# Kernel tuning notes

Measured on AMD Instinct MI355X. Metric: run time of the kernel, lower is better.

Reference implementation:

```python
import jax, jax.numpy as jnp
import numpy as np

E, D, O, G, H, K = 8, 1024, 1024, 512, 2048, 2
B = 8192

def _xavier(key, shape):
    fan_in, fan_out = shape[-2], shape[-1]
    lim = float(np.sqrt(6.0 / (fan_in + fan_out)))
    return jax.random.uniform(key, shape, jnp.float32, -lim, lim)

def setup_inputs() -> dict:
    key = jax.random.key(0)
    ks = jax.random.split(key, 6)
    x = jax.random.normal(ks[0], (B, D), jnp.float32)
    # stacked expert params (xavier-uniform weights, zero bias like torch init)
    W1 = _xavier(ks[1], (E, D, H))
    b1 = jnp.zeros((E, H), jnp.float32)
    W2 = _xavier(ks[2], (E, H, O))
    b2 = jnp.zeros((E, O), jnp.float32)
    # gate params
    Wg1 = _xavier(ks[3], (D, G))
    bg1 = jnp.zeros((G,), jnp.float32)
    Wg2 = _xavier(ks[4], (G, E))
    bg2 = jnp.zeros((E,), jnp.float32)
    return {"x": x, "W1": W1, "b1": b1, "W2": W2, "b2": b2,
            "Wg1": Wg1, "bg1": bg1, "Wg2": Wg2, "bg2": bg2}

def reference(x, W1, b1, W2, b2, Wg1, bg1, Wg2, bg2):
    batch = x.shape[0]
    # gate (dropout inactive in eval)
    gate_logits = jax.nn.relu(x @ Wg1 + bg1) @ Wg2 + bg2          # [B,E]
    gate_scores = jax.nn.softmax(gate_logits, axis=1)
    top_k_scores, top_k_indices = jax.lax.top_k(gate_scores, K)   # [B,K]
    # dense all-expert MLP (mirrors torch.stack over experts)
    h = jax.nn.relu(jnp.einsum('bd,edh->ebh', x, W1) + b1[:, None, :])   # [E,B,H]
    expert_outputs = jnp.einsum('ebh,eho->beo', h, W2) + b2[None, :, :]  # [B,E,O]
    # gather top-k expert outputs, scale, combine
    selected = jnp.take_along_axis(expert_outputs, top_k_indices[:, :, None], axis=1)  # [B,K,O]
    scaled = selected * top_k_scores[:, :, None]
    scaled = scaled / (jnp.sum(top_k_scores, axis=1, keepdims=True)[:, :, None] + 1e-9)
    combined = jnp.sum(scaled, axis=1)                            # [B,O]
    # auxiliary loss
    one_hot = jax.nn.one_hot(top_k_indices, E, dtype=jnp.float32) # [B,K,E]
    expert_load = jnp.sum(one_hot, axis=(0, 1)) / (batch + 1e-9)
    load_balancing_loss = jnp.var(expert_load, ddof=1)            # torch var is unbiased
    entropy = -jnp.mean(jnp.sum(gate_scores * jnp.log(gate_scores + 1e-9), axis=1))
    aux_loss = load_balancing_loss + entropy
    return combined, aux_loss
```

## Files before the change

### kernel.cpp

```cpp
#include <hip/hip_runtime.h>

#define B_ 8192
#define D_ 1024
#define O_ 1024
#define G_ 512
#define H_ 2048
#define E_ 8
#define ROWSP (B_ * 2 + E_ * 128)
#define TAU 0.01f

typedef unsigned short u16;
using f32x4 = __attribute__((ext_vector_type(4))) float;
using s16x8 = __attribute__((ext_vector_type(8))) short;

__device__ __forceinline__ u16 f2bf(float f) {
  union { float f; unsigned u; } v; v.f = f;
  unsigned r = v.u + 0x7FFFu + ((v.u >> 16) & 1u);
  return (u16)(r >> 16);
}
__device__ __forceinline__ float bf2f(u16 h) {
  union { unsigned u; float f; } v; v.u = ((unsigned)h) << 16; return v.f;
}
__device__ __forceinline__ void gload16(const void* g, void* l) {
  __builtin_amdgcn_global_load_lds(
      (const __attribute__((address_space(1))) unsigned int*)g,
      (__attribute__((address_space(3))) unsigned int*)l, 16, 0, 0);
}
__device__ __forceinline__ int xcd_swz(int bid, int nwg) {
  return (bid & 7) * (nwg >> 3) + (bid >> 3);
}
__device__ __forceinline__ int stage_kc(int t) {
  return (((t & 3) ^ ((t >> 3) & 3)) * 8);
}
__device__ __forceinline__ int frag_idx(int lane, int i) {
  int row = i * 16 + (lane & 15);
  int s = (lane >> 4) ^ ((lane >> 1) & 3);
  return (row * 4 + s) * 8;
}

#define PREP_CAST_BLK (B_ * D_ / 4 / 256)
#define PREP_WG1_BLK  ((G_ / 32) * (D_ / 32))
#define PREP_W1_BLK   ((H_ / 32) * (D_ / 32) * E_)
#define PREP_W2_BLK   ((O_ / 32) * (H_ / 32) * E_)

__device__ __forceinline__ void tr_cast_tile(const float* __restrict__ src,
                                             u16* __restrict__ dhi,
                                             u16* __restrict__ dlo,
                                             int R, int C, int bx, int by,
                                             float (*tile)[33], int t) {
  int tx = t & 31, ty = t >> 5;
  int c0 = bx * 32, r0 = by * 32;
#pragma unroll
  for (int p = 0; p < 4; ++p) {
    int r = ty + p * 8;
    tile[r][tx] = src[(size_t)(r0 + r) * C + c0 + tx];
  }
  __syncthreads();
#pragma unroll
  for (int p = 0; p < 4; ++p) {
    int r = ty + p * 8;
    float v = tile[tx][r];
    size_t o = (size_t)(c0 + r) * R + r0 + tx;
    dhi[o] = f2bf(v);
    if (dlo) dlo[o] = f2bf(v - bf2f(f2bf(v)));
  }
}

__global__ __launch_bounds__(256) void k_prep(const float* __restrict__ x,
                                              u16* __restrict__ xhi, u16* __restrict__ xlo,
                                              const float* __restrict__ Wg1,
                                              u16* __restrict__ wg1h, u16* __restrict__ wg1l,
                                              const float* __restrict__ W1, u16* __restrict__ w1t,
                                              const float* __restrict__ W2, u16* __restrict__ w2t) {
  __shared__ float tile[32][33];
  int t = threadIdx.x;
  int b = blockIdx.x;
  if (b < PREP_CAST_BLK) {
    int i = b * 256 + t;
    float4 v = ((const float4*)x)[i];
    u16 h0 = f2bf(v.x), h1 = f2bf(v.y), h2 = f2bf(v.z), h3 = f2bf(v.w);
    ushort4 hi; hi.x = h0; hi.y = h1; hi.z = h2; hi.w = h3;
    ushort4 lo;
    lo.x = f2bf(v.x - bf2f(h0)); lo.y = f2bf(v.y - bf2f(h1));
    lo.z = f2bf(v.z - bf2f(h2)); lo.w = f2bf(v.w - bf2f(h3));
    ((ushort4*)xhi)[i] = hi; ((ushort4*)xlo)[i] = lo;
    return;
  }
  b -= PREP_CAST_BLK;
  if (b < PREP_WG1_BLK) {
    tr_cast_tile(Wg1, wg1h, wg1l, D_, G_, b & 15, b >> 4, tile, t);
    return;
  }
  b -= PREP_WG1_BLK;
  if (b < PREP_W1_BLK) {
    int e = b >> 11, rr = b & 2047;
    size_t ofs = (size_t)e * D_ * H_;
    tr_cast_tile(W1 + ofs, w1t + ofs, nullptr, D_, H_, rr & 63, rr >> 6, tile, t);
    return;
  }
  b -= PREP_W1_BLK;
  {
    int e = b >> 11, rr = b & 2047;
    size_t ofs = (size_t)e * H_ * O_;
    tr_cast_tile(W2 + ofs, w2t + ofs, nullptr, H_, O_, rr & 31, rr >> 5, tile, t);
  }
}

__global__ __launch_bounds__(256) void k_gate_gemm1(const u16* __restrict__ xhi,
                                                    const u16* __restrict__ xlo,
                                                    const u16* __restrict__ whi,
                                                    const u16* __restrict__ wlo,
                                                    const float* __restrict__ bg1,
                                                    float* __restrict__ G1) {
  __shared__ u16 Ah[4096], Al[4096], Bh[4096], Bl[4096];
  int work = xcd_swz(blockIdx.x, (G_ / 128) * (B_ / 128));
  int m0 = (work >> 2) * 128, n0 = (work & 3) * 128;
  int t = threadIdx.x;
  int wave = t >> 6, lane = t & 63;
  int wm = wave >> 1, wn = wave & 1;

  const f32x4 z = {0.f, 0.f, 0.f, 0.f};
  f32x4 acc[4][4];
#pragma unroll
  for (int i = 0; i < 4; ++i)
#pragma unroll
    for (int j = 0; j < 4; ++j) acc[i][j] = z;

  int ar = t >> 2, ac = stage_kc(t);
  const u16* xh0 = xhi + (size_t)(m0 + ar) * D_ + ac;
  const u16* xh1 = xhi + (size_t)(m0 + 64 + ar) * D_ + ac;
  const u16* xl0 = xlo + (size_t)(m0 + ar) * D_ + ac;
  const u16* xl1 = xlo + (size_t)(m0 + 64 + ar) * D_ + ac;
  const u16* wh0 = whi + (size_t)(n0 + ar) * D_ + ac;
  const u16* wh1 = whi + (size_t)(n0 + 64 + ar) * D_ + ac;
  const u16* wl0 = wlo + (size_t)(n0 + ar) * D_ + ac;
  const u16* wl1 = wlo + (size_t)(n0 + 64 + ar) * D_ + ac;

  for (int k0 = 0; k0 < D_; k0 += 32) {
    gload16(xh0 + k0, &Ah[t * 8]); gload16(xh1 + k0, &Ah[2048 + t * 8]);
    gload16(xl0 + k0, &Al[t * 8]); gload16(xl1 + k0, &Al[2048 + t * 8]);
    gload16(wh0 + k0, &Bh[t * 8]); gload16(wh1 + k0, &Bh[2048 + t * 8]);
    gload16(wl0 + k0, &Bl[t * 8]); gload16(wl1 + k0, &Bl[2048 + t * 8]);
    __syncthreads();
    s16x8 ah[4], al[4], bh[4], bl[4];
#pragma unroll
    for (int i = 0; i < 4; ++i) {
      ah[i] = *(const s16x8*)&Ah[wm * 2048 + frag_idx(lane, i)];
      al[i] = *(const s16x8*)&Al[wm * 2048 + frag_idx(lane, i)];
      bh[i] = *(const s16x8*)&Bh[wn * 2048 + frag_idx(lane, i)];
      bl[i] = *(const s16x8*)&Bl[wn * 2048 + frag_idx(lane, i)];
    }
#pragma unroll
    for (int i = 0; i < 4; ++i)
#pragma unroll
      for (int j = 0; j < 4; ++j) {
        acc[i][j] = __builtin_amdgcn_mfma_f32_16x16x32_bf16(ah[i], bh[j], acc[i][j], 0, 0, 0);
        acc[i][j] = __builtin_amdgcn_mfma_f32_16x16x32_bf16(ah[i], bl[j], acc[i][j], 0, 0, 0);
        acc[i][j] = __builtin_amdgcn_mfma_f32_16x16x32_bf16(al[i], bh[j], acc[i][j], 0, 0, 0);
      }
    __syncthreads();
  }
#pragma unroll
  for (int j = 0; j < 4; ++j) {
    int col = n0 + wn * 64 + j * 16 + (lane & 15);
    float bias = bg1[col];
#pragma unroll
    for (int i = 0; i < 4; ++i)
#pragma unroll
      for (int q = 0; q < 4; ++q) {
        int row = m0 + wm * 64 + i * 16 + (lane >> 4) * 4 + q;
        float v = acc[i][j][q] + bias;
        G1[(size_t)row * G_ + col] = v > 0.f ? v : 0.f;
      }
  }
}

__global__ __launch_bounds__(256) void k_gate_logits(const float* __restrict__ G1,
                                                     const float* __restrict__ Wg2,
                                                     const float* __restrict__ bg2,
                                                     float* __restrict__ logits,
                                                     int* __restrict__ flaglist,
                                                     int* __restrict__ nflag) {
  int t = threadIdx.x, wave = t >> 6, lane = t & 63;
  int row = blockIdx.x * 4 + wave;

  float4 g0 = *(const float4*)(G1 + (size_t)row * G_ + lane * 8);
  float4 g1 = *(const float4*)(G1 + (size_t)row * G_ + lane * 8 + 4);
  float g[8] = {g0.x, g0.y, g0.z, g0.w, g1.x, g1.y, g1.z, g1.w};
  float p[8] = {0, 0, 0, 0, 0, 0, 0, 0};
#pragma unroll
  for (int cc = 0; cc < 8; ++cc) {
    int c = lane * 8 + cc;
    float4 w0 = *(const float4*)(Wg2 + c * 8);
    float4 w1 = *(const float4*)(Wg2 + c * 8 + 4);
    p[0] += g[cc] * w0.x; p[1] += g[cc] * w0.y; p[2] += g[cc] * w0.z; p[3] += g[cc] * w0.w;
    p[4] += g[cc] * w1.x; p[5] += g[cc] * w1.y; p[6] += g[cc] * w1.z; p[7] += g[cc] * w1.w;
  }
#pragma unroll
  for (int off = 32; off >= 1; off >>= 1)
#pragma unroll
    for (int e = 0; e < 8; ++e) p[e] += __shfl_xor(p[e], off);
  if (lane == 0) {
    float l1 = -1e30f, l2 = -1e30f, l3 = -1e30f;
#pragma unroll
    for (int e = 0; e < 8; ++e) {
      float v = p[e] + bg2[e];
      logits[(size_t)row * 8 + e] = v;
      if (v > l1) { l3 = l2; l2 = l1; l1 = v; }
      else if (v > l2) { l3 = l2; l2 = v; }
      else if (v > l3) { l3 = v; }
    }
    if (l2 - l3 < TAU) {
      int pos = atomicAdd(nflag, 1);
      flaglist[pos] = row;
    }
  }
}

__global__ __launch_bounds__(256) void k_gate_fixup(const float* __restrict__ x,
                                                    const float* __restrict__ Wg1,
                                                    const float* __restrict__ bg1,
                                                    const float* __restrict__ Wg2,
                                                    const float* __restrict__ bg2,
                                                    const int* __restrict__ flaglist,
                                                    const int* __restrict__ nflag,
                                                    float* __restrict__ logits) {
  __shared__ float xs[1024];
  __shared__ float red[256][9];
  int t = threadIdx.x;
  int n = *nflag;
  for (int i = blockIdx.x; i < n; i += gridDim.x) {
    int row = flaglist[i];
    ((float4*)xs)[t] = ((const float4*)(x + (size_t)row * D_))[t];
    __syncthreads();
    int c0 = t * 2;
    float h0 = 0.f, h1 = 0.f;
#pragma unroll 8
    for (int d = 0; d < D_; ++d) {
      float xv = xs[d];
      float2 w = *(const float2*)(Wg1 + (size_t)d * G_ + c0);
      h0 += xv * w.x; h1 += xv * w.y;
    }
    h0 += bg1[c0]; h1 += bg1[c0 + 1];
    h0 = h0 > 0.f ? h0 : 0.f; h1 = h1 > 0.f ? h1 : 0.f;
#pragma unroll
    for (int e = 0; e < 8; ++e)
      red[t][e] = h0 * Wg2[c0 * 8 + e] + h1 * Wg2[(c0 + 1) * 8 + e];
    __syncthreads();
    for (int s = 128; s >= 1; s >>= 1) {
      if (t < s) {
#pragma unroll
        for (int e = 0; e < 8; ++e) red[t][e] += red[t + s][e];
      }
      __syncthreads();
    }
    if (t < 8) logits[(size_t)row * 8 + t] = red[0][t] + bg2[t];
    __syncthreads();
  }
}

__global__ __launch_bounds__(256) void k_gate_final(const float* __restrict__ logits,
                                                    int* __restrict__ topidx,
                                                    float* __restrict__ wnorm,
                                                    int* __restrict__ counts,
                                                    float* __restrict__ entacc) {
  __shared__ int cnt_s[8];
  __shared__ float ent_s[4];
  int t = threadIdx.x;
  if (t < 8) cnt_s[t] = 0;
  __syncthreads();
  int row = blockIdx.x * 256 + t;
  float4 a = ((const float4*)logits)[(size_t)row * 2];
  float4 b = ((const float4*)logits)[(size_t)row * 2 + 1];
  float L[8] = {a.x, a.y, a.z, a.w, b.x, b.y, b.z, b.w};
  float m = L[0];
#pragma unroll
  for (int e = 1; e < 8; ++e) m = fmaxf(m, L[e]);
  float s[8], Z = 0.f;
#pragma unroll
  for (int e = 0; e < 8; ++e) { s[e] = expf(L[e] - m); Z += s[e]; }
  float inv = 1.f / Z;
  float sc[8];
#pragma unroll
  for (int e = 0; e < 8; ++e) sc[e] = s[e] * inv;
  int i1 = 0;
#pragma unroll
  for (int e = 1; e < 8; ++e) if (L[e] > L[i1]) i1 = e;
  int i2 = (i1 == 0) ? 1 : 0;
#pragma unroll
  for (int e = 0; e < 8; ++e) if (e != i1 && L[e] > L[i2]) i2 = e;
  float s1 = sc[i1], s2 = sc[i2];
  float denom = s1 + s2 + 1e-9f;
  topidx[row * 2] = i1; topidx[row * 2 + 1] = i2;
  wnorm[row * 2] = s1 / denom; wnorm[row * 2 + 1] = s2 / denom;
  atomicAdd(&cnt_s[i1], 1); atomicAdd(&cnt_s[i2], 1);
  float ent = 0.f;
#pragma unroll
  for (int e = 0; e < 8; ++e) ent -= sc[e] * logf(sc[e] + 1e-9f);
#pragma unroll
  for (int off = 32; off >= 1; off >>= 1) ent += __shfl_xor(ent, off);
  if ((t & 63) == 0) ent_s[t >> 6] = ent;
  __syncthreads();
  if (t == 0) atomicAdd(entacc, ent_s[0] + ent_s[1] + ent_s[2] + ent_s[3]);
  if (t < 8) atomicAdd(&counts[t], cnt_s[t]);
}

__global__ void k_scan(const int* __restrict__ counts, const float* __restrict__ entacc,
                       int* __restrict__ aoff, float* __restrict__ aux_out) {
  if (threadIdx.x == 0 && blockIdx.x == 0) {
    int off = 0; aoff[0] = 0;
    float ld[8]; float mean = 0.f;
    for (int e = 0; e < 8; ++e) {
      ld[e] = (float)counts[e] / (8192.0f + 1e-9f);
      mean += ld[e];
      off += ((counts[e] + 127) >> 7) << 7;
      aoff[e + 1] = off;
    }
    mean *= 0.125f;
    float var = 0.f;
    for (int e = 0; e < 8; ++e) { float d = ld[e] - mean; var += d * d; }
    var *= (1.0f / 7.0f);
    *aux_out = var + entacc[0] / 8192.0f;
  }
}

__global__ __launch_bounds__(256) void k_scatter(const int* __restrict__ topidx,
                                                 const float* __restrict__ wnorm,
                                                 const int* __restrict__ aoff,
                                                 int* __restrict__ fill,
                                                 int* __restrict__ tok_list,
                                                 float* __restrict__ wroute,
                                                 int* __restrict__ pos_of) {
  int t = blockIdx.x * 256 + threadIdx.x;
  if (t >= B_ * 2) return;
  int e = topidx[t];
  int pos = aoff[e] + atomicAdd(&fill[e], 1);
  tok_list[pos] = t >> 1;
  wroute[pos] = wnorm[t];
  pos_of[t] = pos;
}


__global__ __launch_bounds__(256) void k_egemm1(const u16* __restrict__ xhi,
                                                const u16* __restrict__ w1t,
                                                const float* __restrict__ b1v,
                                                const int* __restrict__ tok_list,
                                                const int* __restrict__ aoff,
                                                u16* __restrict__ hbuf) {
  __shared__ u16 As[2][4096], Bs[2][2048];
  int work = xcd_swz(blockIdx.x, (ROWSP / 128) * (H_ / 64));
  int rt = work >> 5;
  int n0 = (work & 31) * 64;
  int row0 = rt * 128;
  if (row0 >= aoff[8]) return;
  int e = 0;
  while (row0 >= aoff[e + 1]) ++e;
  int t = threadIdx.x, wave = t >> 6, lane = t & 63;
  int wm = wave >> 1, wn = wave & 1;
  const u16* w1e = w1t + (size_t)e * H_ * D_;

  int ar = t >> 2, ac = stage_kc(t);
  int tok0 = tok_list[row0 + ar];       if ((unsigned)tok0 >= B_) tok0 = 0;
  int tok1 = tok_list[row0 + 64 + ar];  if ((unsigned)tok1 >= B_) tok1 = 0;
  const u16* a0 = xhi + (size_t)tok0 * D_ + ac;
  const u16* a1 = xhi + (size_t)tok1 * D_ + ac;
  const u16* bb = w1e + (size_t)(n0 + ar) * D_ + ac;

  const f32x4 z = {0.f, 0.f, 0.f, 0.f};
  f32x4 acc[4][2];
#pragma unroll
  for (int i = 0; i < 4; ++i)
#pragma unroll
    for (int j = 0; j < 2; ++j) acc[i][j] = z;

  gload16(a0, &As[0][t * 8]);
  gload16(a1, &As[0][2048 + t * 8]);
  gload16(bb, &Bs[0][t * 8]);
  __syncthreads();

  const int NT = D_ / 32;
  for (int kt = 0; kt < NT; ++kt) {
    int cur = kt & 1, nxt = cur ^ 1;
    if (kt + 1 < NT) {
      int kk = (kt + 1) * 32;
      gload16(a0 + kk, &As[nxt][t * 8]);
      gload16(a1 + kk, &As[nxt][2048 + t * 8]);
      gload16(bb + kk, &Bs[nxt][t * 8]);
    }
    s16x8 af[4], bf[2];
#pragma unroll
    for (int i = 0; i < 4; ++i)
      af[i] = *(const s16x8*)&As[cur][wm * 2048 + frag_idx(lane, i)];
#pragma unroll
    for (int j = 0; j < 2; ++j)
      bf[j] = *(const s16x8*)&Bs[cur][frag_idx(lane, wn * 2 + j)];
#pragma unroll
    for (int i = 0; i < 4; ++i)
#pragma unroll
      for (int j = 0; j < 2; ++j)
        acc[i][j] = __builtin_amdgcn_mfma_f32_16x16x32_bf16(af[i], bf[j], acc[i][j], 0, 0, 0);
    __syncthreads();
  }
#pragma unroll
  for (int j = 0; j < 2; ++j) {
    int col = n0 + wn * 32 + j * 16 + (lane & 15);
    float bias = b1v[e * H_ + col];
#pragma unroll
    for (int i = 0; i < 4; ++i)
#pragma unroll
      for (int q = 0; q < 4; ++q) {
        int row = row0 + wm * 64 + i * 16 + (lane >> 4) * 4 + q;
        float v = acc[i][j][q] + bias;
        hbuf[(size_t)row * H_ + col] = f2bf(v > 0.f ? v : 0.f);
      }
  }
}

__global__ __launch_bounds__(256) void k_egemm2(const u16* __restrict__ hbuf,
                                                const u16* __restrict__ w2t,
                                                const float* __restrict__ b2v,
                                                const int* __restrict__ aoff,
                                                const float* __restrict__ wroute,
                                                u16* __restrict__ rbuf) {
  __shared__ u16 As[2][4096], Bs[2][2048];
  int work = xcd_swz(blockIdx.x, (ROWSP / 128) * (O_ / 64));
  int rt = work >> 4;
  int n0 = (work & 15) * 64;
  int row0 = rt * 128;
  if (row0 >= aoff[8]) return;
  int e = 0;
  while (row0 >= aoff[e + 1]) ++e;
  int t = threadIdx.x, wave = t >> 6, lane = t & 63;
  int wm = wave >> 1, wn = wave & 1;
  const u16* w2e = w2t + (size_t)e * O_ * H_;

  int ar = t >> 2, ac = stage_kc(t);
  const u16* a0 = hbuf + (size_t)(row0 + ar) * H_ + ac;
  const u16* a1 = hbuf + (size_t)(row0 + 64 + ar) * H_ + ac;
  const u16* bb = w2e + (size_t)(n0 + ar) * H_ + ac;

  const f32x4 z = {0.f, 0.f, 0.f, 0.f};
  f32x4 acc[4][2];
#pragma unroll
  for (int i = 0; i < 4; ++i)
#pragma unroll
    for (int j = 0; j < 2; ++j) acc[i][j] = z;

  gload16(a0, &As[0][t * 8]);
  gload16(a1, &As[0][2048 + t * 8]);
  gload16(bb, &Bs[0][t * 8]);
  __syncthreads();

  const int NT = H_ / 32;
  for (int kt = 0; kt < NT; ++kt) {
    int cur = kt & 1, nxt = cur ^ 1;
    if (kt + 1 < NT) {
      int kk = (kt + 1) * 32;
      gload16(a0 + kk, &As[nxt][t * 8]);
      gload16(a1 + kk, &As[nxt][2048 + t * 8]);
      gload16(bb + kk, &Bs[nxt][t * 8]);
    }
    s16x8 af[4], bf[2];
#pragma unroll
    for (int i = 0; i < 4; ++i)
      af[i] = *(const s16x8*)&As[cur][wm * 2048 + frag_idx(lane, i)];
#pragma unroll
    for (int j = 0; j < 2; ++j)
      bf[j] = *(const s16x8*)&Bs[cur][frag_idx(lane, wn * 2 + j)];
#pragma unroll
    for (int i = 0; i < 4; ++i)
#pragma unroll
      for (int j = 0; j < 2; ++j)
        acc[i][j] = __builtin_amdgcn_mfma_f32_16x16x32_bf16(af[i], bf[j], acc[i][j], 0, 0, 0);
    __syncthreads();
  }
#pragma unroll
  for (int i = 0; i < 4; ++i)
#pragma unroll
    for (int q = 0; q < 4; ++q) {
      int row = row0 + wm * 64 + i * 16 + (lane >> 4) * 4 + q;
      float wv = wroute[row];
#pragma unroll
      for (int j = 0; j < 2; ++j) {
        int col = n0 + wn * 32 + j * 16 + (lane & 15);
        float bias = b2v[e * O_ + col];
        rbuf[(size_t)row * O_ + col] = f2bf((acc[i][j][q] + bias) * wv);
      }
    }
}

__global__ __launch_bounds__(256) void k_combine(const u16* __restrict__ rbuf,
                                                 const int* __restrict__ pos_of,
                                                 float* __restrict__ out) {
  int t = threadIdx.x;
  int tok = blockIdx.x * 2 + (t >> 7);
  int c = (t & 127) * 8;
  int p0 = pos_of[tok * 2], p1 = pos_of[tok * 2 + 1];
  const u16* r0 = rbuf + (size_t)p0 * O_ + c;
  const u16* r1 = rbuf + (size_t)p1 * O_ + c;
  ushort4 a0 = *(const ushort4*)r0, a1 = *(const ushort4*)(r0 + 4);
  ushort4 b0 = *(const ushort4*)r1, b1 = *(const ushort4*)(r1 + 4);
  float4 o0, o1;
  o0.x = bf2f(a0.x) + bf2f(b0.x); o0.y = bf2f(a0.y) + bf2f(b0.y);
  o0.z = bf2f(a0.z) + bf2f(b0.z); o0.w = bf2f(a0.w) + bf2f(b0.w);
  o1.x = bf2f(a1.x) + bf2f(b1.x); o1.y = bf2f(a1.y) + bf2f(b1.y);
  o1.z = bf2f(a1.z) + bf2f(b1.z); o1.w = bf2f(a1.w) + bf2f(b1.w);
  float* op = out + (size_t)tok * O_ + c;
  *(float4*)op = o0; *(float4*)(op + 4) = o1;
}

static const size_t o_xhi  = 0;
static const size_t o_xlo  = o_xhi + (size_t)B_ * D_ * 2;
static const size_t o_w1t  = o_xlo + (size_t)B_ * D_ * 2;
static const size_t o_w2t  = o_w1t + (size_t)E_ * H_ * D_ * 2;
static const size_t o_wg1h = o_w2t + (size_t)E_ * O_ * H_ * 2;
static const size_t o_wg1l = o_wg1h + (size_t)G_ * D_ * 2;
static const size_t o_G1   = o_wg1l + (size_t)G_ * D_ * 2;
static const size_t o_h    = o_G1 + (size_t)B_ * G_ * 4;
static const size_t o_idx  = o_h + (size_t)ROWSP * H_ * 2;
static const size_t o_wn   = o_idx + (size_t)B_ * 2 * 4;
static const size_t o_pos  = o_wn + (size_t)B_ * 2 * 4;
static const size_t o_tok  = o_pos + (size_t)B_ * 2 * 4;
static const size_t o_wr   = o_tok + (size_t)ROWSP * 4;
static const size_t o_cnt  = o_wr + (size_t)ROWSP * 4;
static const size_t o_fill = o_cnt + 32;
static const size_t o_ent  = o_cnt + 64;
static const size_t o_nfl  = o_cnt + 96;
static const size_t o_aoff = o_cnt + 128;
static const size_t o_logits = o_cnt + 256;
static const size_t o_flag   = o_logits + (size_t)B_ * 8 * 4;
static const size_t o_rbuf = o_xlo;

extern "C" void kernel_launch(void* const* d_in, const int* in_sizes, int n_in,
                              void* d_out, int out_size, void* d_ws, size_t ws_size,
                              hipStream_t stream) {
  const float* x   = (const float*)d_in[0];
  const float* W1  = (const float*)d_in[1];
  const float* b1  = (const float*)d_in[2];
  const float* W2  = (const float*)d_in[3];
  const float* b2  = (const float*)d_in[4];
  const float* Wg1 = (const float*)d_in[5];
  const float* bg1 = (const float*)d_in[6];
  const float* Wg2 = (const float*)d_in[7];
  const float* bg2 = (const float*)d_in[8];
  float* out = (float*)d_out;
  char* ws = (char*)d_ws;

  u16* xhi  = (u16*)(ws + o_xhi);
  u16* xlo  = (u16*)(ws + o_xlo);
  u16* w1t  = (u16*)(ws + o_w1t);
  u16* w2t  = (u16*)(ws + o_w2t);
  u16* wg1h = (u16*)(ws + o_wg1h);
  u16* wg1l = (u16*)(ws + o_wg1l);
  float* G1 = (float*)(ws + o_G1);
  u16* hbuf = (u16*)(ws + o_h);
  int* topidx = (int*)(ws + o_idx);
  float* wnorm = (float*)(ws + o_wn);
  int* pos_of = (int*)(ws + o_pos);
  int* tok_list = (int*)(ws + o_tok);
  float* wroute = (float*)(ws + o_wr);
  int* counts = (int*)(ws + o_cnt);
  int* fill = (int*)(ws + o_fill);
  float* entacc = (float*)(ws + o_ent);
  int* nflag = (int*)(ws + o_nfl);
  int* aoff = (int*)(ws + o_aoff);
  float* logits = (float*)(ws + o_logits);
  int* flaglist = (int*)(ws + o_flag);
  u16* rbuf = (u16*)(ws + o_rbuf);

  hipMemsetAsync(ws + o_cnt, 0, 128, stream);

  k_prep<<<PREP_CAST_BLK + PREP_WG1_BLK + PREP_W1_BLK + PREP_W2_BLK, 256, 0, stream>>>(
      x, xhi, xlo, Wg1, wg1h, wg1l, W1, w1t, W2, w2t);

  k_gate_gemm1<<<(G_ / 128) * (B_ / 128), 256, 0, stream>>>(xhi, xlo, wg1h, wg1l, bg1, G1);
  k_gate_logits<<<B_ / 4, 256, 0, stream>>>(G1, Wg2, bg2, logits, flaglist, nflag);
  k_gate_fixup<<<128, 256, 0, stream>>>(x, Wg1, bg1, Wg2, bg2, flaglist, nflag, logits);
  k_gate_final<<<B_ / 256, 256, 0, stream>>>(logits, topidx, wnorm, counts, entacc);
  k_scan<<<1, 64, 0, stream>>>(counts, entacc, aoff, out + (size_t)B_ * O_);
  k_scatter<<<(B_ * 2) / 256, 256, 0, stream>>>(topidx, wnorm, aoff, fill, tok_list, wroute, pos_of);

  k_egemm1<<<(ROWSP / 128) * (H_ / 64), 256, 0, stream>>>(xhi, w1t, b1, tok_list, aoff, hbuf);
  k_egemm2<<<(ROWSP / 128) * (O_ / 64), 256, 0, stream>>>(hbuf, w2t, b2, aoff, wroute, rbuf);
  k_combine<<<B_ / 2, 256, 0, stream>>>(rbuf, pos_of, out);
}
```

Before: 552.5 us.

## Enlarge expert GEMM tiles to 128x128 and switch to 32x32x16 MFMA

Both expert GEMMs move from 128x64 to 128x128 output tiles. Each wave now computes a 64x64 block with 32x32x16 bf16 MFMA instructions instead of 16x16x32 ones, using a new swizzled fragment index for LDS reads. The larger tile halves the grid and cuts repeated A-operand (gathered activations) traffic per output, and the larger MFMA shape needs fewer LDS fragment reads per FLOP. In exchange it uses more LDS and more accumulator registers per thread, and there are fewer blocks to fill the CUs.

```diff
diff --git a/kernel.cpp b/kernel.cpp
--- a/kernel.cpp
+++ b/kernel.cpp
@@ -10,8 +10,9 @@
 #define TAU 0.01f
 
 typedef unsigned short u16;
-using f32x4 = __attribute__((ext_vector_type(4))) float;
-using s16x8 = __attribute__((ext_vector_type(8))) short;
+using f32x4  = __attribute__((ext_vector_type(4))) float;
+using f32x16 = __attribute__((ext_vector_type(16))) float;
+using s16x8  = __attribute__((ext_vector_type(8))) short;
 
 __device__ __forceinline__ u16 f2bf(float f) {
   union { float f; unsigned u; } v; v.f = f;
@@ -36,6 +37,11 @@
   int row = i * 16 + (lane & 15);
   int s = (lane >> 4) ^ ((lane >> 1) & 3);
   return (row * 4 + s) * 8;
+}
+__device__ __forceinline__ int fidx32(int lane, int mi, int kh) {
+  int r = mi * 32 + (lane & 31);
+  int s = (kh * 2 + (lane >> 5)) ^ ((r >> 1) & 3);
+  return (r * 4 + s) * 8;
 }
 
 #define PREP_CAST_BLK (B_ * D_ / 4 / 256)
@@ -347,10 +353,10 @@
                                                 const int* __restrict__ tok_list,
                                                 const int* __restrict__ aoff,
                                                 u16* __restrict__ hbuf) {
-  __shared__ u16 As[2][4096], Bs[2][2048];
-  int work = xcd_swz(blockIdx.x, (ROWSP / 128) * (H_ / 64));
-  int rt = work >> 5;
-  int n0 = (work & 31) * 64;
+  __shared__ u16 As[2][4096], Bs[2][4096];
+  int work = xcd_swz(blockIdx.x, (H_ / 128) * (ROWSP / 128));
+  int rt = work >> 4;
+  int n0 = (work & 15) * 128;
   int row0 = rt * 128;
   if (row0 >= aoff[8]) return;
   int e = 0;
@@ -364,18 +370,19 @@
   int tok1 = tok_list[row0 + 64 + ar];  if ((unsigned)tok1 >= B_) tok1 = 0;
   const u16* a0 = xhi + (size_t)tok0 * D_ + ac;
   const u16* a1 = xhi + (size_t)tok1 * D_ + ac;
-  const u16* bb = w1e + (size_t)(n0 + ar) * D_ + ac;
-
-  const f32x4 z = {0.f, 0.f, 0.f, 0.f};
-  f32x4 acc[4][2];
-#pragma unroll
-  for (int i = 0; i < 4; ++i)
-#pragma unroll
-    for (int j = 0; j < 2; ++j) acc[i][j] = z;
-
-  gload16(a0, &As[0][t * 8]);
-  gload16(a1, &As[0][2048 + t * 8]);
-  gload16(bb, &Bs[0][t * 8]);
+  const u16* bb0 = w1e + (size_t)(n0 + ar) * D_ + ac;
+  const u16* bb1 = w1e + (size_t)(n0 + 64 + ar) * D_ + ac;
+
+  f32x16 acc[2][2];
+#pragma unroll
+  for (int i = 0; i < 2; ++i)
+#pragma unroll
+    for (int j = 0; j < 2; ++j)
+#pragma unroll
+      for (int q = 0; q < 16; ++q) acc[i][j][q] = 0.f;
+
+  gload16(a0, &As[0][t * 8]);  gload16(a1, &As[0][2048 + t * 8]);
+  gload16(bb0, &Bs[0][t * 8]); gload16(bb1, &Bs[0][2048 + t * 8]);
   __syncthreads();
 
   const int NT = D_ / 32;
@@ -383,34 +390,36 @@
     int cur = kt & 1, nxt = cur ^ 1;
     if (kt + 1 < NT) {
       int kk = (kt + 1) * 32;
-      gload16(a0 + kk, &As[nxt][t * 8]);
-      gload16(a1 + kk, &As[nxt][2048 + t * 8]);
-      gload16(bb + kk, &Bs[nxt][t * 8]);
-    }
-    s16x8 af[4], bf[2];
-#pragma unroll
-    for (int i = 0; i < 4; ++i)
-      af[i] = *(const s16x8*)&As[cur][wm * 2048 + frag_idx(lane, i)];
-#pragma unroll
-    for (int j = 0; j < 2; ++j)
-      bf[j] = *(const s16x8*)&Bs[cur][frag_idx(lane, wn * 2 + j)];
-#pragma unroll
-    for (int i = 0; i < 4; ++i)
-#pragma unroll
-      for (int j = 0; j < 2; ++j)
-        acc[i][j] = __builtin_amdgcn_mfma_f32_16x16x32_bf16(af[i], bf[j], acc[i][j], 0, 0, 0);
-    __syncthreads();
-  }
-#pragma unroll
-  for (int j = 0; j < 2; ++j) {
-    int col = n0 + wn * 32 + j * 16 + (lane & 15);
+      gload16(a0 + kk, &As[nxt][t * 8]);  gload16(a1 + kk, &As[nxt][2048 + t * 8]);
+      gload16(bb0 + kk, &Bs[nxt][t * 8]); gload16(bb1 + kk, &Bs[nxt][2048 + t * 8]);
+    }
+    s16x8 af[2][2], bf[2][2];
+#pragma unroll
+    for (int mi = 0; mi < 2; ++mi)
+#pragma unroll
+      for (int kh = 0; kh < 2; ++kh) {
+        af[mi][kh] = *(const s16x8*)&As[cur][wm * 2048 + fidx32(lane, mi, kh)];
+        bf[mi][kh] = *(const s16x8*)&Bs[cur][wn * 2048 + fidx32(lane, mi, kh)];
+      }
+#pragma unroll
+    for (int mi = 0; mi < 2; ++mi)
+#pragma unroll
+      for (int nj = 0; nj < 2; ++nj) {
+        acc[mi][nj] = __builtin_amdgcn_mfma_f32_32x32x16_bf16(af[mi][0], bf[nj][0], acc[mi][nj], 0, 0, 0);
+        acc[mi][nj] = __builtin_amdgcn_mfma_f32_32x32x16_bf16(af[mi][1], bf[nj][1], acc[mi][nj], 0, 0, 0);
+      }
+    __syncthreads();
+  }
+#pragma unroll
+  for (int nj = 0; nj < 2; ++nj) {
+    int col = n0 + wn * 64 + nj * 32 + (lane & 31);
     float bias = b1v[e * H_ + col];
 #pragma unroll
-    for (int i = 0; i < 4; ++i)
-#pragma unroll
-      for (int q = 0; q < 4; ++q) {
-        int row = row0 + wm * 64 + i * 16 + (lane >> 4) * 4 + q;
-        float v = acc[i][j][q] + bias;
+    for (int mi = 0; mi < 2; ++mi)
+#pragma unroll
+      for (int r = 0; r < 16; ++r) {
+        int row = row0 + wm * 64 + mi * 32 + (r & 3) + 8 * (r >> 2) + 4 * (lane >> 5);
+        float v = acc[mi][nj][r] + bias;
         hbuf[(size_t)row * H_ + col] = f2bf(v > 0.f ? v : 0.f);
       }
   }
@@ -422,10 +431,10 @@
                                                 const int* __restrict__ aoff,
                                                 const float* __restrict__ wroute,
                                                 u16* __restrict__ rbuf) {
-  __shared__ u16 As[2][4096], Bs[2][2048];
-  int work = xcd_swz(blockIdx.x, (ROWSP / 128) * (O_ / 64));
-  int rt = work >> 4;
-  int n0 = (work & 15) * 64;
+  __shared__ u16 As[2][4096], Bs[2][4096];
+  int work = xcd_swz(blockIdx.x, (O_ / 128) * (ROWSP / 128));
+  int rt = work >> 3;
+  int n0 = (work & 7) * 128;
   int row0 = rt * 128;
   if (row0 >= aoff[8]) return;
   int e = 0;
@@ -437,18 +446,19 @@
   int ar = t >> 2, ac = stage_kc(t);
   const u16* a0 = hbuf + (size_t)(row0 + ar) * H_ + ac;
   const u16* a1 = hbuf + (size_t)(row0 + 64 + ar) * H_ + ac;
-  const u16* bb = w2e + (size_t)(n0 + ar) * H_ + ac;
-
-  const f32x4 z = {0.f, 0.f, 0.f, 0.f};
-  f32x4 acc[4][2];
-#pragma unroll
-  for (int i = 0; i < 4; ++i)
-#pragma unroll
-    for (int j = 0; j < 2; ++j) acc[i][j] = z;
-
-  gload16(a0, &As[0][t * 8]);
-  gload16(a1, &As[0][2048 + t * 8]);
-  gload16(bb, &Bs[0][t * 8]);
+  const u16* bb0 = w2e + (size_t)(n0 + ar) * H_ + ac;
+  const u16* bb1 = w2e + (size_t)(n0 + 64 + ar) * H_ + ac;
+
+  f32x16 acc[2][2];
+#pragma unroll
+  for (int i = 0; i < 2; ++i)
+#pragma unroll
+    for (int j = 0; j < 2; ++j)
+#pragma unroll
+      for (int q = 0; q < 16; ++q) acc[i][j][q] = 0.f;
+
+  gload16(a0, &As[0][t * 8]);  gload16(a1, &As[0][2048 + t * 8]);
+  gload16(bb0, &Bs[0][t * 8]); gload16(bb1, &Bs[0][2048 + t * 8]);
   __syncthreads();
 
   const int NT = H_ / 32;
@@ -456,35 +466,37 @@
     int cur = kt & 1, nxt = cur ^ 1;
     if (kt + 1 < NT) {
       int kk = (kt + 1) * 32;
-      gload16(a0 + kk, &As[nxt][t * 8]);
-      gload16(a1 + kk, &As[nxt][2048 + t * 8]);
-      gload16(bb + kk, &Bs[nxt][t * 8]);
-    }
-    s16x8 af[4], bf[2];
-#pragma unroll
-    for (int i = 0; i < 4; ++i)
-      af[i] = *(const s16x8*)&As[cur][wm * 2048 + frag_idx(lane, i)];
-#pragma unroll
-    for (int j = 0; j < 2; ++j)
-      bf[j] = *(const s16x8*)&Bs[cur][frag_idx(lane, wn * 2 + j)];
-#pragma unroll
-    for (int i = 0; i < 4; ++i)
-#pragma unroll
-      for (int j = 0; j < 2; ++j)
-        acc[i][j] = __builtin_amdgcn_mfma_f32_16x16x32_bf16(af[i], bf[j], acc[i][j], 0, 0, 0);
-    __syncthreads();
-  }
-#pragma unroll
-  for (int i = 0; i < 4; ++i)
-#pragma unroll
-    for (int q = 0; q < 4; ++q) {
-      int row = row0 + wm * 64 + i * 16 + (lane >> 4) * 4 + q;
+      gload16(a0 + kk, &As[nxt][t * 8]);  gload16(a1 + kk, &As[nxt][2048 + t * 8]);
+      gload16(bb0 + kk, &Bs[nxt][t * 8]); gload16(bb1 + kk, &Bs[nxt][2048 + t * 8]);
+    }
+    s16x8 af[2][2], bf[2][2];
+#pragma unroll
+    for (int mi = 0; mi < 2; ++mi)
+#pragma unroll
+      for (int kh = 0; kh < 2; ++kh) {
+        af[mi][kh] = *(const s16x8*)&As[cur][wm * 2048 + fidx32(lane, mi, kh)];
+        bf[mi][kh] = *(const s16x8*)&Bs[cur][wn * 2048 + fidx32(lane, mi, kh)];
+      }
+#pragma unroll
+    for (int mi = 0; mi < 2; ++mi)
+#pragma unroll
+      for (int nj = 0; nj < 2; ++nj) {
+        acc[mi][nj] = __builtin_amdgcn_mfma_f32_32x32x16_bf16(af[mi][0], bf[nj][0], acc[mi][nj], 0, 0, 0);
+        acc[mi][nj] = __builtin_amdgcn_mfma_f32_32x32x16_bf16(af[mi][1], bf[nj][1], acc[mi][nj], 0, 0, 0);
+      }
+    __syncthreads();
+  }
+#pragma unroll
+  for (int mi = 0; mi < 2; ++mi)
+#pragma unroll
+    for (int r = 0; r < 16; ++r) {
+      int row = row0 + wm * 64 + mi * 32 + (r & 3) + 8 * (r >> 2) + 4 * (lane >> 5);
       float wv = wroute[row];
 #pragma unroll
-      for (int j = 0; j < 2; ++j) {
-        int col = n0 + wn * 32 + j * 16 + (lane & 15);
+      for (int nj = 0; nj < 2; ++nj) {
+        int col = n0 + wn * 64 + nj * 32 + (lane & 31);
         float bias = b2v[e * O_ + col];
-        rbuf[(size_t)row * O_ + col] = f2bf((acc[i][j][q] + bias) * wv);
+        rbuf[(size_t)row * O_ + col] = f2bf((acc[mi][nj][r] + bias) * wv);
       }
     }
 }
@@ -580,7 +592,7 @@
   k_scan<<<1, 64, 0, stream>>>(counts, entacc, aoff, out + (size_t)B_ * O_);
   k_scatter<<<(B_ * 2) / 256, 256, 0, stream>>>(topidx, wnorm, aoff, fill, tok_list, wroute, pos_of);
 
-  k_egemm1<<<(ROWSP / 128) * (H_ / 64), 256, 0, stream>>>(xhi, w1t, b1, tok_list, aoff, hbuf);
-  k_egemm2<<<(ROWSP / 128) * (O_ / 64), 256, 0, stream>>>(hbuf, w2t, b2, aoff, wroute, rbuf);
+  k_egemm1<<<(H_ / 128) * (ROWSP / 128), 256, 0, stream>>>(xhi, w1t, b1, tok_list, aoff, hbuf);
+  k_egemm2<<<(O_ / 128) * (ROWSP / 128), 256, 0, stream>>>(hbuf, w2t, b2, aoff, wroute, rbuf);
   k_combine<<<B_ / 2, 256, 0, stream>>>(rbuf, pos_of, out);
 }
```

New measurement: 506.8 us. 1.09x faster.
